# Kernel tuning notes

Measured on AMD Instinct MI355X. Metric: run time of the kernel, lower is better.

## Reference

```python
import jax, jax.numpy as jnp
import numpy as np

S, N, M = 8, 4096, 64          # snapshots, atoms, total neighbors (sum of max_num_neighs)
L = 20.0                        # periodic box length
R_CS, R_C = 2.0, 6.0            # smooth cutoff radii
DSUB = 16                       # dim_sub_net
PAD_FRAC = 0.15                 # fraction of -1 padded neighbor slots


def _mlp(x, params):
    # DenseChainNet: Linear -> relu between layers, no activation after last layer
    n = len(params)
    for i, (W, b) in enumerate(params):
        x = x @ W + b
        if i < n - 1:
            x = jax.nn.relu(x)
    return x


def _lin(k, fan_in, fan_out):
    k1, k2 = jax.random.split(k)
    s = 1.0 / np.sqrt(fan_in)
    W = jax.random.uniform(k1, (fan_in, fan_out), minval=-s, maxval=s, dtype=jnp.float32)
    b = jax.random.uniform(k2, (fan_out,), minval=-s, maxval=s, dtype=jnp.float32)
    return W, b


def setup_inputs() -> dict:
    key = jax.random.key(0)
    ks = jax.random.split(key, 12)
    inputs = jax.random.uniform(ks[0], (S, N, 3), dtype=jnp.float32) * L
    input_types = jax.random.randint(ks[1], (S, N), 0, 2)
    # neighbor indices, guaranteed != self, with -1 padding
    base = jnp.arange(N, dtype=jnp.int32)[None, :, None]
    off = jax.random.randint(ks[2], (S, N, M), 1, N)
    neigh = (base + off) % N
    pad = jax.random.uniform(ks[3], (S, N, M)) < PAD_FRAC
    neigh_list = jnp.where(pad, -1, neigh).astype(jnp.int32)
    es1_w, es1_b = _lin(ks[4], 2, 4)
    es2_w, es2_b = _lin(ks[5], 4, 4)
    fs1_w, fs1_b = _lin(ks[6], 4, 4)
    fs2_w, fs2_b = _lin(ks[7], 4, 4)
    en1_w, en1_b = _lin(ks[8], 4, 8)
    en2_w, en2_b = _lin(ks[9], 8, 16)
    en3_w, en3_b = _lin(ks[10], 16, 32)
    return dict(inputs=inputs, input_types=input_types, neigh_list=neigh_list,
                es1_w=es1_w, es1_b=es1_b, es2_w=es2_w, es2_b=es2_b,
                fs1_w=fs1_w, fs1_b=fs1_b, fs2_w=fs2_w, fs2_b=fs2_b,
                en1_w=en1_w, en1_b=en1_b, en2_w=en2_w, en2_b=en2_b,
                en3_w=en3_w, en3_b=en3_b)


def reference(inputs, input_types, neigh_list,
              es1_w, es1_b, es2_w, es2_b,
              fs1_w, fs1_b, fs2_w, fs2_b,
              en1_w, en1_b, en2_w, en2_b, en3_w, en3_b):
    mask = neigh_list == -1                               # [S,N,M]
    idx = jnp.where(mask, 0, neigh_list)
    flat = idx.reshape(S, N * M)
    # gather neighbor coordinates with periodic minimum-image convention
    pos_j = jnp.take_along_axis(inputs, flat[..., None], axis=1).reshape(S, N, M, 3)
    d = pos_j - inputs[:, :, None, :]
    d = d - L * jnp.round(d / L)
    r = jnp.sqrt(jnp.sum(d * d, axis=-1) + 1e-12)         # [S,N,M]
    # smooth cutoff: s(r) = 1/r for r<r_cs, cosine switch to 0 at r_c
    u = (r - R_CS) / (R_C - R_CS)
    sw = jnp.where(r < R_CS, 1.0,
                   jnp.where(r < R_C, 0.5 * jnp.cos(jnp.pi * u) + 0.5, 0.0))
    s_ij = jnp.where(mask, 0.0, sw / r)                   # [S,N,M]
    r_ij = d * (s_ij / r)[..., None]                      # s(r) * d / r, [S,N,M,3]
    # species pair descriptor (symmetrized over pair order)
    neigh_types = jnp.take_along_axis(input_types, flat, axis=1).reshape(S, N, M)
    self_t = jnp.broadcast_to(input_types[:, :, None], (S, N, M))
    pairs = jnp.stack([self_t, neigh_types], axis=-1).astype(jnp.float32).reshape(-1, 2)
    es = [(es1_w, es1_b), (es2_w, es2_b)]
    td = _mlp(pairs, es) + _mlp(pairs[:, ::-1], es)
    td = _mlp(td, [(fs1_w, fs1_b), (fs2_w, fs2_b)]).reshape(S, N, M, -1)  # [S,N,M,4]
    s_tilde = (td * s_ij[..., None]).reshape(S * N * M, -1)
    G = _mlp(s_tilde, [(en1_w, en1_b), (en2_w, en2_b), (en3_w, en3_b)]).reshape(S, N, M, -1)  # [S,N,M,32]
    r_tilde = jnp.concatenate([s_ij[..., None], r_ij], axis=-1)            # [S,N,M,4]
    R = jnp.einsum('snmd,snmk->sndk', r_tilde, G[..., :DSUB])              # [S,N,4,16]
    R1 = jnp.einsum('snmd,sndk->snmk', r_tilde, R)                         # [S,N,M,16]
    D = jnp.einsum('snmg,snmk->sngk', G, R1)                               # [S,N,32,16]
    return D
```

## Files before the change

### kernel.cpp

```cpp
#include <hip/hip_runtime.h>
#include <math.h>

#define SS 8
#define NN 4096
#define MM 64
#define LBOX 20.0f

typedef __attribute__((ext_vector_type(8)))  short    short8;
typedef __attribute__((ext_vector_type(2)))  float    floatx2;
typedef __attribute__((ext_vector_type(4)))  float    floatx4;
typedef __attribute__((ext_vector_type(2)))  __bf16   bf16x2;

__device__ inline unsigned pkbf(float a, float b) {
    bf16x2 p; p.x = (__bf16)a; p.y = (__bf16)b;
    unsigned u; __builtin_memcpy(&u, &p, 4); return u;
}

#define WS_POSW   0
#define WS_WT     (524288 / 4)
#define WT_VT     0
#define WT_B3P    32
#define WT_W3P    64

__global__ __launch_bounds__(256) void prep_kernel(
    const float* __restrict__ pos, const int* __restrict__ types,
    const float* __restrict__ es1_w, const float* __restrict__ es1_b,
    const float* __restrict__ es2_w, const float* __restrict__ es2_b,
    const float* __restrict__ fs1_w, const float* __restrict__ fs1_b,
    const float* __restrict__ fs2_w, const float* __restrict__ fs2_b,
    const float* __restrict__ en1_w, const float* __restrict__ en3_w,
    const float* __restrict__ en3_b, float* __restrict__ ws)
{
    const int tid = threadIdx.x;
    const int b = blockIdx.x;
    if (b < 128) {
        const int i = b * 256 + tid;
        floatx4 v;
        v.x = pos[i * 3 + 0];
        v.y = pos[i * 3 + 1];
        v.z = pos[i * 3 + 2];
        v.w = __int_as_float(types[i]);
        *((floatx4*)ws + i) = v;
        return;
    }
    float* wt = ws + WS_WT;
    if (tid < 4) {
        const float ti = (float)(tid >> 1), tj = (float)(tid & 1);
        float e[4] = {0.f, 0.f, 0.f, 0.f};
        #pragma unroll
        for (int swp = 0; swp < 2; ++swp) {
            const float a = swp ? tj : ti, bb = swp ? ti : tj;
            float h[4];
            #pragma unroll
            for (int k = 0; k < 4; ++k)
                h[k] = fmaxf(a * es1_w[k] + bb * es1_w[4 + k] + es1_b[k], 0.f);
            #pragma unroll
            for (int k = 0; k < 4; ++k) {
                float acc = es2_b[k];
                #pragma unroll
                for (int j = 0; j < 4; ++j) acc += h[j] * es2_w[j * 4 + k];
                e[k] += acc;
            }
        }
        float f[4];
        #pragma unroll
        for (int k = 0; k < 4; ++k) {
            float acc = fs1_b[k];
            #pragma unroll
            for (int j = 0; j < 4; ++j) acc += e[j] * fs1_w[j * 4 + k];
            f[k] = fmaxf(acc, 0.f);
        }
        float td[4];
        #pragma unroll
        for (int k = 0; k < 4; ++k) {
            float acc = fs2_b[k];
            #pragma unroll
            for (int j = 0; j < 4; ++j) acc += f[j] * fs2_w[j * 4 + k];
            td[k] = acc;
        }
        #pragma unroll
        for (int o = 0; o < 8; ++o) {
            float acc = 0.f;
            #pragma unroll
            for (int d = 0; d < 4; ++d) acc += td[d] * en1_w[d * 8 + o];
            wt[WT_VT + tid * 8 + o] = acc;
        }
    }
    if (tid < 32)
        wt[WT_B3P + tid] = en3_b[(tid & 1) * 16 + (tid >> 1)];
    #pragma unroll
    for (int rr = 0; rr < 2; ++rr) {
        const int i = tid + rr * 256;
        const int hp = i >> 6, g = (i >> 2) & 15, w = i & 3;
        wt[WT_W3P + i] = en3_w[(2 * hp + (w >> 1)) * 32 + g + 16 * (w & 1)];
    }
}

__global__ __launch_bounds__(256) void desc_kernel(
    const float* __restrict__ ws,
    const int*   __restrict__ neigh,
    const float* __restrict__ en1_b,
    const float* __restrict__ en2_w, const float* __restrict__ en2_b,
    float* __restrict__ out)
{
    __shared__ alignas(16) unsigned short sh_h2[4][16][72];
    __shared__ alignas(16) unsigned short sh_rt[4][4][72];
    __shared__ alignas(16) float sh_PT[4][4][20];
    __shared__ alignas(16) float sh_W3p[512];
    __shared__ alignas(16) float sh_b3p[16][2];
    __shared__ alignas(16) float sh_A[4][128];
    __shared__ alignas(16) float sh_vt[4][8];

    const int tid = threadIdx.x;
    const float* wt = ws + WS_WT;

    if (tid < 32) {
        ((float*)sh_vt)[tid]  = wt[WT_VT + tid];
        ((float*)sh_b3p)[tid] = wt[WT_B3P + tid];
    }
    sh_W3p[tid]       = wt[WT_W3P + tid];
    sh_W3p[tid + 256] = wt[WT_W3P + 256 + tid];
    __syncthreads();

    const int wave = __builtin_amdgcn_readfirstlane(tid >> 6);
    const int lane = tid & 63;
    const int atom = __builtin_amdgcn_readfirstlane(blockIdx.x * 4 + (tid >> 6));
    const int sbase = atom & ~(NN - 1);
    const floatx4* __restrict__ pw = (const floatx4*)ws;

    const floatx4 pi4 = pw[atom];
    const float xi = pi4.x, yi = pi4.y, zi = pi4.z;
    const int   ti = __float_as_int(pi4.w);

    const int nb  = neigh[atom * MM + lane];
    const int msk = nb < 0;
    const int gj  = sbase + (msk ? 0 : nb);
    const floatx4 pj4 = pw[gj];
    const int tj = __float_as_int(pj4.w);

    float dx = pj4.x - xi;
    float dy = pj4.y - yi;
    float dz = pj4.z - zi;
    dx -= LBOX * rintf(dx * (1.0f / LBOX));
    dy -= LBOX * rintf(dy * (1.0f / LBOX));
    dz -= LBOX * rintf(dz * (1.0f / LBOX));
    const float r2   = fmaf(dx, dx, fmaf(dy, dy, fmaf(dz, dz, 1e-12f)));
    const float rinv = rsqrtf(r2);
    const float r    = r2 * rinv;
    const float u    = fminf(fmaxf((r - 2.0f) * 0.25f, 0.0f), 1.0f);
    const float swv  = 0.5f * __cosf(3.14159265358979323846f * u) + 0.5f;
    const float sij   = msk ? 0.0f : swv * rinv;
    const float scale = sij * rinv;
    const int   tt    = ti * 2 + tj;

    float h1[8];
    {
        const float4 va = *(const float4*)(&sh_vt[tt][0]);
        const float4 vb = *(const float4*)(&sh_vt[tt][4]);
        h1[0] = fmaxf(fmaf(sij, va.x, en1_b[0]), 0.f);
        h1[1] = fmaxf(fmaf(sij, va.y, en1_b[1]), 0.f);
        h1[2] = fmaxf(fmaf(sij, va.z, en1_b[2]), 0.f);
        h1[3] = fmaxf(fmaf(sij, va.w, en1_b[3]), 0.f);
        h1[4] = fmaxf(fmaf(sij, vb.x, en1_b[4]), 0.f);
        h1[5] = fmaxf(fmaf(sij, vb.y, en1_b[5]), 0.f);
        h1[6] = fmaxf(fmaf(sij, vb.z, en1_b[6]), 0.f);
        h1[7] = fmaxf(fmaf(sij, vb.w, en1_b[7]), 0.f);
    }

    #pragma unroll
    for (int k = 0; k < 16; ++k) {
        float acc = en2_b[k];
        #pragma unroll
        for (int i = 0; i < 8; ++i) acc = fmaf(h1[i], en2_w[i * 16 + k], acc);
        sh_h2[wave][k][lane] = (unsigned short)pkbf(fmaxf(acc, 0.f), 0.f);
    }
    {
        const unsigned p0 = pkbf(sij, dx * scale), p1 = pkbf(dy * scale, dz * scale);
        sh_rt[wave][0][lane] = (unsigned short)p0;
        sh_rt[wave][1][lane] = (unsigned short)(p0 >> 16);
        sh_rt[wave][2][lane] = (unsigned short)p1;
        sh_rt[wave][3][lane] = (unsigned short)(p1 >> 16);
    }
    asm volatile("s_waitcnt lgkmcnt(0)" ::: "memory");

    const int col16 = lane & 15;
    const int q4    = lane >> 4;
    const int m0    = q4 * 8;
    floatx4 cP = {0.f, 0.f, 0.f, 0.f};
    floatx4 cQ = {0.f, 0.f, 0.f, 0.f};
    const short8 ones = (short8)(short)0x3F80;
    #pragma unroll
    for (int ck = 0; ck < 2; ++ck) {
        const short8 af = *(const short8*)&sh_h2[wave][col16][ck * 32 + m0];
        const short8 bf = *(const short8*)&sh_rt[wave][col16 & 3][ck * 32 + m0];
        cP = __builtin_amdgcn_mfma_f32_16x16x32_bf16(af, bf, cP, 0, 0, 0);
        cQ = __builtin_amdgcn_mfma_f32_16x16x32_bf16(ones, bf, cQ, 0, 0, 0);
    }
    if (col16 < 4) *(floatx4*)&sh_PT[wave][col16][q4 * 4] = cP;
    const float qd = cQ[0];
    asm volatile("s_waitcnt lgkmcnt(0)" ::: "memory");

    {
        const int g0 = lane >> 2, dd = lane & 3;
        const floatx2 b3v = *(const floatx2*)&sh_b3p[g0][0];
        floatx2 acc2 = floatx2{qd, qd} * b3v;
        #pragma unroll
        for (int h4 = 0; h4 < 4; ++h4) {
            const floatx4 pv = *(const floatx4*)&sh_PT[wave][dd][h4 * 4];
            const floatx4 wa = *(const floatx4*)&sh_W3p[(h4 * 2 + 0) * 64 + g0 * 4];
            const floatx4 wb = *(const floatx4*)&sh_W3p[(h4 * 2 + 1) * 64 + g0 * 4];
            acc2 += floatx2{pv.x, pv.x} * floatx2{wa.x, wa.y};
            acc2 += floatx2{pv.y, pv.y} * floatx2{wa.z, wa.w};
            acc2 += floatx2{pv.z, pv.z} * floatx2{wb.x, wb.y};
            acc2 += floatx2{pv.w, pv.w} * floatx2{wb.z, wb.w};
        }
        sh_A[wave][lane]      = acc2.x;
        sh_A[wave][lane + 64] = acc2.y;
    }
    asm volatile("s_waitcnt lgkmcnt(0)" ::: "memory");

    {
        const int g = lane >> 1, koff = (lane & 1) * 8;
        const floatx4 Ag = *(const floatx4*)&sh_A[wave][g * 4];
        floatx4 o0, o1;
        #pragma unroll
        for (int jj = 0; jj < 8; ++jj) {
            const floatx4 Ak = *(const floatx4*)&sh_A[wave][(koff + jj) * 4];
            const float v = fmaf(Ag.x, Ak.x, fmaf(Ag.y, Ak.y, fmaf(Ag.z, Ak.z, Ag.w * Ak.w)));
            if (jj < 4) o0[jj] = v; else o1[jj - 4] = v;
        }
        float* op = out + (size_t)atom * 512 + lane * 8;
        __builtin_nontemporal_store(o0, (floatx4*)op);
        __builtin_nontemporal_store(o1, (floatx4*)(op + 4));
    }
}

extern "C" void kernel_launch(void* const* d_in, const int* in_sizes, int n_in,
                              void* d_out, int out_size, void* d_ws, size_t ws_size,
                              hipStream_t stream) {
    const float* pos   = (const float*)d_in[0];
    const int*   typ   = (const int*)d_in[1];
    const int*   ngh   = (const int*)d_in[2];
    float* ws = (float*)d_ws;

    prep_kernel<<<dim3(129), dim3(256), 0, stream>>>(
        pos, typ,
        (const float*)d_in[3],  (const float*)d_in[4],
        (const float*)d_in[5],  (const float*)d_in[6],
        (const float*)d_in[7],  (const float*)d_in[8],
        (const float*)d_in[9],  (const float*)d_in[10],
        (const float*)d_in[11],
        (const float*)d_in[15], (const float*)d_in[16],
        ws);

    desc_kernel<<<dim3((SS * NN) / 4), dim3(256), 0, stream>>>(
        ws, ngh,
        (const float*)d_in[12],
        (const float*)d_in[13], (const float*)d_in[14],
        (float*)d_out);
}
```

Before: 125.9 us.

## Compute the en3 projection and final Gram product with bf16 MFMA instead of scalar FMA

Replaces the scalar LDS-staged loops for the last linear layer (P times W3 plus bias) and the final A·Aᵀ descriptor product with two pairs of 16x16x16 bf16 MFMA instructions. W3 is pre-packed into bf16 MFMA fragments in the prep kernel, and the intermediate A matrix is stored in LDS as bf16. This removes several LDS round trips and many VALU FMAs per atom. In exchange it rounds the intermediates P and A to bf16, which adds error, and the output stores become scalar 4-byte writes instead of 16-byte vector writes.

```diff
diff --git a/kernel.cpp b/kernel.cpp
--- a/kernel.cpp
+++ b/kernel.cpp
@@ -7,8 +7,9 @@
 #define LBOX 20.0f
 
 typedef __attribute__((ext_vector_type(8)))  short    short8;
-typedef __attribute__((ext_vector_type(2)))  float    floatx2;
+typedef __attribute__((ext_vector_type(4)))  short    s16x4;
 typedef __attribute__((ext_vector_type(4)))  float    floatx4;
+typedef __attribute__((ext_vector_type(2)))  unsigned uintx2;
 typedef __attribute__((ext_vector_type(2)))  __bf16   bf16x2;
 
 __device__ inline unsigned pkbf(float a, float b) {
@@ -16,11 +17,26 @@
     unsigned u; __builtin_memcpy(&u, &p, 4); return u;
 }
 
+#if defined(__has_builtin)
+#  if __has_builtin(__builtin_amdgcn_mfma_f32_16x16x16bf16_1k)
+#    define MFMA16(a,b,c) __builtin_amdgcn_mfma_f32_16x16x16bf16_1k(a,b,c,0,0,0)
+#  endif
+#endif
+#ifndef MFMA16
+static __device__ inline floatx4 mfma16_asm(s16x4 a, s16x4 b, floatx4 c) {
+    floatx4 d;
+    asm("v_mfma_f32_16x16x16_bf16 %0, %1, %2, %3\n\ts_nop 7\n\ts_nop 7"
+        : "=v"(d) : "v"(a), "v"(b), "v"(c));
+    return d;
+}
+#  define MFMA16(a,b,c) mfma16_asm(a,b,c)
+#endif
+
 #define WS_POSW   0
 #define WS_WT     (524288 / 4)
 #define WT_VT     0
-#define WT_B3P    32
-#define WT_W3P    64
+#define WT_B3     32
+#define WT_W3F    64
 
 __global__ __launch_bounds__(256) void prep_kernel(
     const float* __restrict__ pos, const int* __restrict__ types,
@@ -87,12 +103,17 @@
         }
     }
     if (tid < 32)
-        wt[WT_B3P + tid] = en3_b[(tid & 1) * 16 + (tid >> 1)];
-    #pragma unroll
-    for (int rr = 0; rr < 2; ++rr) {
-        const int i = tid + rr * 256;
-        const int hp = i >> 6, g = (i >> 2) & 15, w = i & 3;
-        wt[WT_W3P + i] = en3_w[(2 * hp + (w >> 1)) * 32 + g + 16 * (w & 1)];
+        wt[WT_B3 + tid] = en3_b[tid];
+    if (tid < 128) {
+        const int half = tid >> 6, l = tid & 63;
+        const int q4 = l >> 4, col = l & 15;
+        const int gg = half * 16 + col;
+        float v0 = en3_w[(q4 * 4 + 0) * 32 + gg];
+        float v1 = en3_w[(q4 * 4 + 1) * 32 + gg];
+        float v2 = en3_w[(q4 * 4 + 2) * 32 + gg];
+        float v3 = en3_w[(q4 * 4 + 3) * 32 + gg];
+        uintx2 pk; pk.x = pkbf(v0, v1); pk.y = pkbf(v2, v3);
+        ((uintx2*)(wt + WT_W3F))[tid] = pk;
     }
 }
 
@@ -105,21 +126,20 @@
 {
     __shared__ alignas(16) unsigned short sh_h2[4][16][72];
     __shared__ alignas(16) unsigned short sh_rt[4][4][72];
-    __shared__ alignas(16) float sh_PT[4][4][20];
-    __shared__ alignas(16) float sh_W3p[512];
-    __shared__ alignas(16) float sh_b3p[16][2];
-    __shared__ alignas(16) float sh_A[4][128];
     __shared__ alignas(16) float sh_vt[4][8];
+    __shared__ alignas(16) float sh_b3[32];
+    __shared__ alignas(16) unsigned sh_w3f[2][64][2];
+    __shared__ alignas(16) unsigned short sh_Ab[4][32][4];
 
     const int tid = threadIdx.x;
     const float* wt = ws + WS_WT;
 
     if (tid < 32) {
-        ((float*)sh_vt)[tid]  = wt[WT_VT + tid];
-        ((float*)sh_b3p)[tid] = wt[WT_B3P + tid];
-    }
-    sh_W3p[tid]       = wt[WT_W3P + tid];
-    sh_W3p[tid + 256] = wt[WT_W3P + 256 + tid];
+        ((float*)sh_vt)[tid] = wt[WT_VT + tid];
+        sh_b3[tid]           = wt[WT_B3 + tid];
+    }
+    if (tid < 128)
+        ((uintx2*)sh_w3f)[tid] = ((const uintx2*)(wt + WT_W3F))[tid];
     __syncthreads();
 
     const int wave = __builtin_amdgcn_readfirstlane(tid >> 6);
@@ -196,42 +216,40 @@
         cP = __builtin_amdgcn_mfma_f32_16x16x32_bf16(af, bf, cP, 0, 0, 0);
         cQ = __builtin_amdgcn_mfma_f32_16x16x32_bf16(ones, bf, cQ, 0, 0, 0);
     }
-    if (col16 < 4) *(floatx4*)&sh_PT[wave][col16][q4 * 4] = cP;
+
+    s16x4 pfrag;
+    {
+        const unsigned p0 = pkbf(cP[0], cP[1]), p1 = pkbf(cP[2], cP[3]);
+        unsigned* pp = (unsigned*)&pfrag; pp[0] = p0; pp[1] = p1;
+    }
     const float qd = cQ[0];
+    const s16x4 w3f0 = *(const s16x4*)&sh_w3f[0][lane][0];
+    const s16x4 w3f1 = *(const s16x4*)&sh_w3f[1][lane][0];
+    const floatx4 b3v0 = *(const floatx4*)&sh_b3[q4 * 4];
+    const floatx4 b3v1 = *(const floatx4*)&sh_b3[16 + q4 * 4];
+    const floatx4 cA0 = MFMA16(w3f0, pfrag, b3v0 * qd);
+    const floatx4 cA1 = MFMA16(w3f1, pfrag, b3v1 * qd);
+
+    if (col16 < 4) {
+        #pragma unroll
+        for (int j = 0; j < 4; ++j) {
+            sh_Ab[wave][q4 * 4 + j][col16]      = (unsigned short)pkbf(cA0[j], 0.f);
+            sh_Ab[wave][16 + q4 * 4 + j][col16] = (unsigned short)pkbf(cA1[j], 0.f);
+        }
+    }
     asm volatile("s_waitcnt lgkmcnt(0)" ::: "memory");
-
-    {
-        const int g0 = lane >> 2, dd = lane & 3;
-        const floatx2 b3v = *(const floatx2*)&sh_b3p[g0][0];
-        floatx2 acc2 = floatx2{qd, qd} * b3v;
-        #pragma unroll
-        for (int h4 = 0; h4 < 4; ++h4) {
-            const floatx4 pv = *(const floatx4*)&sh_PT[wave][dd][h4 * 4];
-            const floatx4 wa = *(const floatx4*)&sh_W3p[(h4 * 2 + 0) * 64 + g0 * 4];
-            const floatx4 wb = *(const floatx4*)&sh_W3p[(h4 * 2 + 1) * 64 + g0 * 4];
-            acc2 += floatx2{pv.x, pv.x} * floatx2{wa.x, wa.y};
-            acc2 += floatx2{pv.y, pv.y} * floatx2{wa.z, wa.w};
-            acc2 += floatx2{pv.z, pv.z} * floatx2{wb.x, wb.y};
-            acc2 += floatx2{pv.w, pv.w} * floatx2{wb.z, wb.w};
-        }
-        sh_A[wave][lane]      = acc2.x;
-        sh_A[wave][lane + 64] = acc2.y;
-    }
-    asm volatile("s_waitcnt lgkmcnt(0)" ::: "memory");
-
-    {
-        const int g = lane >> 1, koff = (lane & 1) * 8;
-        const floatx4 Ag = *(const floatx4*)&sh_A[wave][g * 4];
-        floatx4 o0, o1;
-        #pragma unroll
-        for (int jj = 0; jj < 8; ++jj) {
-            const floatx4 Ak = *(const floatx4*)&sh_A[wave][(koff + jj) * 4];
-            const float v = fmaf(Ag.x, Ak.x, fmaf(Ag.y, Ak.y, fmaf(Ag.z, Ak.z, Ag.w * Ak.w)));
-            if (jj < 4) o0[jj] = v; else o1[jj - 4] = v;
-        }
-        float* op = out + (size_t)atom * 512 + lane * 8;
-        __builtin_nontemporal_store(o0, (floatx4*)op);
-        __builtin_nontemporal_store(o1, (floatx4*)(op + 4));
+    s16x4 fA0 = *(const s16x4*)&sh_Ab[wave][col16][0];
+    s16x4 fA1 = *(const s16x4*)&sh_Ab[wave][16 + col16][0];
+    if (q4 != 0) { fA0 = (s16x4)(short)0; fA1 = (s16x4)(short)0; }
+    const floatx4 zz = {0.f, 0.f, 0.f, 0.f};
+    const floatx4 cD0 = MFMA16(fA0, fA0, zz);
+    const floatx4 cD1 = MFMA16(fA1, fA0, zz);
+
+    float* op = out + (size_t)atom * 512;
+    #pragma unroll
+    for (int j = 0; j < 4; ++j) {
+        __builtin_nontemporal_store(cD0[j], op + (q4 * 4 + j) * 16 + col16);
+        __builtin_nontemporal_store(cD1[j], op + (16 + q4 * 4 + j) * 16 + col16);
     }
 }
 
```

Result: slower. 128.9 us (+2.4%).
